# Optimization experiments

Measured on AMD Instinct MI355X. Metric: run time of the kernel, lower is better.

The kernel has to match this reference:

```python
import jax, jax.numpy as jnp
import numpy as np

EPS = 1e-5
NEG_SLOPE = 0.2
B, C, P, K, E, H = 16, 16, 2048, 16, 64, 2


def cross_set_gather(f, idx):
    # f: (B, C, P), idx: (B, P, K) -> (B, C, P, K)
    return jax.vmap(lambda fb, ib: fb[:, ib])(f, idx)


def bn(x, g, b, m, v, axes):
    # x normalized along channel dim; g,b,m,v shaped to broadcast via `axes` reshape
    return (x - m.reshape(axes)) * (g.reshape(axes) / jnp.sqrt(v.reshape(axes) + EPS)) + b.reshape(axes)


def setup_inputs() -> dict:
    key = jax.random.key(0)
    ks = jax.random.split(key, 16)
    features = jax.random.normal(ks[0], (B, C, P), dtype=jnp.float32)
    neighbor_indices = jax.random.randint(ks[1], (B, P, K), 0, P)
    mask = jax.random.randint(ks[2], (B, 1, P), 0, 2).astype(bool)
    s = 0.1
    return {
        "features": features,
        "neighbor_indices": neighbor_indices,
        "mask": mask,
        "node_w": jax.random.normal(ks[3], (H, E, C)) * s,
        "node_g": jnp.ones((H, E)),
        "node_b": jnp.zeros((H, E)),
        "node_m": jax.random.normal(ks[4], (H, E)) * s,
        "node_v": jax.random.uniform(ks[5], (H, E)) + 0.5,
        "edge_w": jax.random.normal(ks[6], (H, E, C)) * s,
        "edge_bias": jax.random.normal(ks[7], (H, E)) * s,
        "edge_g": jnp.ones((H, E)),
        "edge_b2": jnp.zeros((H, E)),
        "edge_m": jax.random.normal(ks[8], (H, E)) * s,
        "edge_v": jax.random.uniform(ks[9], (H, E)) + 0.5,
        "self_w": jax.random.normal(ks[10], (H, E)) * s,
        "self_b": jax.random.normal(ks[11], (H,)) * s,
        "nb_w": jax.random.normal(ks[12], (H, E)) * s,
        "nb_b": jax.random.normal(ks[13], (H,)) * s,
    }


def _forward(features, neighbor_indices, mask, node_w, node_g, node_b, node_m, node_v,
             edge_w, edge_bias, edge_g, edge_b2, edge_m, edge_v, self_w, self_b, nb_w, nb_b):
    mask_f = mask.astype(features.dtype)  # (B,1,P)
    # node encoding (Conv1d k=1 + BN): (B,H,E,P)
    nodes = jnp.einsum('hec,bcp->bhep', node_w, features)
    nodes = bn(nodes, node_g, node_b, node_m, node_v, (1, H, E, 1))
    # edge features: neighbor - center, (B,C,P,K)
    nbr = cross_set_gather(features, neighbor_indices)
    edge_feat = nbr - features[:, :, :, None]
    # edge encoding (Conv2d k=1 + BN): (B,H,E,P,K)
    enc = jnp.einsum('hec,bcpk->bhepk', edge_w, edge_feat) + edge_bias[None, :, :, None, None]
    enc = bn(enc, edge_g, edge_b2, edge_m, edge_v, (1, H, E, 1, 1))
    # attention scores
    self_score = jnp.einsum('he,bhep->bhp', self_w, nodes) + self_b[None, :, None]  # (B,H,P)
    nb_score = jnp.einsum('he,bhepk->bhpk', nb_w, enc) + nb_b[None, :, None, None]  # (B,H,P,K)
    logits = self_score[..., None] + nb_score
    logits = jnp.where(logits >= 0, logits, NEG_SLOPE * logits)  # leaky_relu(0.2)
    # neighbor validity mask: (B,P,K)
    valid = cross_set_gather(mask_f, neighbor_indices)[:, 0]
    vb = valid[:, None, :, :]  # (B,1,P,K)
    logits = jnp.where(vb == 0, -jnp.inf, logits)
    coef = jnp.nan_to_num(jax.nn.softmax(logits, axis=-1), nan=0.0, posinf=0.0, neginf=0.0)  # (B,H,P,K)
    # weighted aggregation + relu: (B,H,E,P)
    att = jax.nn.relu(jnp.einsum('bhpk,bhepk->bhep', coef, enc))
    # graph features: masked max over K
    enc_masked = jnp.where(vb[:, :, None, :, :] == 0, -jnp.inf, enc)
    graph = jnp.max(enc_masked, axis=-1)  # (B,H,E,P)
    graph = jnp.where(jnp.isinf(graph), 0.0, graph)
    # multi-head combine: element-wise max over heads, then mask
    att_out = jnp.max(att, axis=1) * mask_f  # (B,E,P)
    graph_out = jnp.max(graph, axis=1) * mask_f  # (B,E,P)
    return att_out, graph_out


def reference(features, neighbor_indices, mask, node_w, node_g, node_b, node_m, node_v,
              edge_w, edge_bias, edge_g, edge_b2, edge_m, edge_v, self_w, self_b, nb_w, nb_b):
    return _forward(features, neighbor_indices, mask, node_w, node_g, node_b, node_m, node_v,
                    edge_w, edge_bias, edge_g, edge_b2, edge_m, edge_v, self_w, self_b, nb_w, nb_b)
```

## Files before the change

kernel.cpp:

```cpp
#include <hip/hip_runtime.h>
#include <hip/hip_bf16.h>
#include <hip/hip_fp16.h>
#include <math.h>

#define NB 16
#define NC 16
#define NP 2048
#define NK 16
#define NE 64
#define NH 2
#define EPSV 1e-5f
#define NSLOPE 0.2f
#define QINV -1e30f
#define QTHR -1e29f

#define WS_PINFO 16384
#define WS_EPB   2162688

__device__ __forceinline__ float ldf(const void* p, int i, int isb) {
  return isb ? __bfloat162float(((const __hip_bfloat16*)p)[i]) : ((const float*)p)[i];
}
__device__ __forceinline__ unsigned f2bf(float f) {
  unsigned u = __float_as_uint(f);
  return (u + 0x7FFFu + ((u >> 16) & 1u)) >> 16;
}
__device__ __forceinline__ float bflo(unsigned v) { return __uint_as_float(v << 16); }
__device__ __forceinline__ float bfhi(unsigned v) { return __uint_as_float(v & 0xFFFF0000u); }

__global__ void __launch_bounds__(256) k_proj(
    const void* feat, const void* mask,
    const void* edge_w, const void* node_w,
    const void* edge_g, const void* edge_v,
    const void* node_g, const void* node_v, const void* node_b, const void* node_m,
    const void* self_w, const void* self_b, const void* nb_w,
    char* ws)
{
  __shared__ int sh_isb, sh_mbyte;
  __shared__ float ewl[128*17];
  __shared__ float nwl[128*17];
  __shared__ float fl[NC][64];
  __shared__ float w2[128], wn[128], ctr[128];
  __shared__ float s_wq[32], s_wsc[32], s_cself[2];

  const int tid = threadIdx.x;
  const int w = tid >> 6, lane = tid & 63;

  if (w == 0) {
    const unsigned short* u = (const unsigned short*)feat;
    int cnt = 0;
#pragma unroll
    for (int i = 0; i < 8; i++) {
      int ex = (u[lane*8 + i] >> 7) & 0xFF;
      cnt += (ex >= 100 && ex <= 135) ? 1 : 0;
    }
#pragma unroll
    for (int o = 32; o >= 1; o >>= 1) cnt += __shfl_xor(cnt, o);
    if (lane == 0) sh_isb = (cnt >= 460) ? 1 : 0;
  }
  if (w == 1) {
    const unsigned char* mb = (const unsigned char*)mask;
    int c = 0;
#pragma unroll
    for (int i = 0; i < 16; i++) {
      int ix = lane*16 + i;
      c += ((ix & 3) && mb[ix]) ? 1 : 0;
    }
#pragma unroll
    for (int o = 32; o >= 1; o >>= 1) c += __shfl_xor(c, o);
    if (lane == 0) sh_mbyte = (c > 0) ? 1 : 0;
  }
  __syncthreads();
  const int isb = sh_isb, mbyte = sh_mbyte;

  const int bid = blockIdx.x;
  const int b  = (bid & 7)*2 + ((bid >> 3) & 1);
  const int pt = bid >> 4;
  const int p0 = pt * 64;

  for (int i = tid; i < 128*16; i += 256) {
    const int he = i >> 4, c = i & 15;
    ewl[he*17 + c] = ldf(edge_w, i, isb);
    nwl[he*17 + c] = ldf(node_w, i, isb);
  }
  for (int i = tid; i < NC*64; i += 256) {
    int c = i >> 6, p = i & 63;
    fl[c][p] = ldf(feat, (b*NC + c)*NP + p0 + p, isb);
  }
  if (tid < 128) {
    const int he = tid;
    float se = ldf(edge_g, he, isb) * rsqrtf(ldf(edge_v, he, isb) + EPSV);
    float ns = ldf(node_g, he, isb) * rsqrtf(ldf(node_v, he, isb) + EPSV);
    w2[he]  = ldf(nb_w, he, isb) * se;
    wn[he]  = ldf(self_w, he, isb) * ns;
    ctr[he] = ldf(self_w, he, isb) * (ldf(node_b, he, isb) - ldf(node_m, he, isb) * ns);
  }
  __syncthreads();
  if (tid < 32) {
    const int h = tid >> 4, c = tid & 15;
    float sq = 0.f, sn = 0.f;
#pragma unroll 8
    for (int e = 0; e < NE; e++) {
      sq += w2[h*NE+e] * ewl[(h*NE+e)*17 + c];
      sn += wn[h*NE+e] * nwl[(h*NE+e)*17 + c];
    }
    s_wq[tid]  = sq;
    s_wsc[tid] = sn;
  }
  if (tid < 2) {
    float cs = 0.f;
#pragma unroll 8
    for (int e = 0; e < NE; e++) cs += ctr[tid*NE+e];
    s_cself[tid] = cs + ldf(self_b, tid, isb);
  }
  __syncthreads();

  const int e = tid & 63;
  const int pp = tid >> 6;
  float wv0[NC], wv1[NC];
#pragma unroll
  for (int c = 0; c < NC; c++) {
    wv0[c] = ewl[e*17 + c];
    wv1[c] = ewl[(NE + e)*17 + c];
  }
  unsigned* epb = (unsigned*)(ws + WS_EPB);
  const long base = (long)(b*NP + p0) * 64;
  for (int pass = 0; pass < 16; pass++) {
    const int p = pass*4 + pp;
    float a0 = 0.f, a1 = 0.f;
#pragma unroll
    for (int c = 0; c < NC; c++) {
      const float f = fl[c][p];
      a0 = fmaf(wv0[c], f, a0);
      a1 = fmaf(wv1[c], f, a1);
    }
    epb[base + (long)p*64 + e] = f2bf(a0) | (f2bf(a1) << 16);
  }

  if (tid < 64) {
    float q0=0.f, q1=0.f, s0=0.f, s1=0.f;
#pragma unroll
    for (int c = 0; c < NC; c++) {
      const float f = fl[c][tid];
      q0 = fmaf(s_wq[c],     f, q0);
      q1 = fmaf(s_wq[16+c],  f, q1);
      s0 = fmaf(s_wsc[c],    f, s0);
      s1 = fmaf(s_wsc[16+c], f, s1);
    }
    const int p = p0 + tid;
    bool mv;
    if (mbyte) mv = ((const unsigned char*)mask)[b*NP + p] != 0;
    else       mv = ((const int*)mask)[b*NP + p] != 0;
    float4 pi;
    pi.x = mv ? q0 : QINV;
    pi.y = mv ? q1 : QINV;
    pi.z = s0 + s_cself[0];
    pi.w = s1 + s_cself[1];
    ((float4*)(ws + WS_PINFO))[b*NP + p] = pi;
  }
}

__global__ void __launch_bounds__(256) k_main(
    const void* feat, const int* nidx,
    const void* edge_g, const void* edge_v, const void* edge_bias,
    const void* edge_m, const void* edge_b2,
    const void* nb_w, const void* nb_b,
    char* ws, void* out)
{
  __shared__ int sh_isb;
  __shared__ float sh_se[128], sh_cbe[128], sh_cnb[2];
  __shared__ uint2 ent[32][17];
  __shared__ unsigned char cntcm[32];
  __shared__ float att_t[NE][33];
  __shared__ float gr_t[NE][33];

  const int tid  = threadIdx.x;
  const int w    = tid >> 6;
  const int lane = tid & 63;

  if (w == 0) {
    const unsigned short* u = (const unsigned short*)feat;
    int cnt = 0;
#pragma unroll
    for (int i = 0; i < 8; i++) {
      int ex = (u[lane*8 + i] >> 7) & 0xFF;
      cnt += (ex >= 100 && ex <= 135) ? 1 : 0;
    }
#pragma unroll
    for (int o = 32; o >= 1; o >>= 1) cnt += __shfl_xor(cnt, o);
    if (lane == 0) sh_isb = (cnt >= 460) ? 1 : 0;
  }
  __syncthreads();
  const int isb = sh_isb;

  if (tid < 128) {
    const int he = tid, h = tid >> 6;
    float se = ldf(edge_g, he, isb) * rsqrtf(ldf(edge_v, he, isb) + EPSV);
    float cb = se * (ldf(edge_bias, he, isb) - ldf(edge_m, he, isb)) + ldf(edge_b2, he, isb);
    sh_se[he]  = se;
    sh_cbe[he] = cb;
    float t = ldf(nb_w, he, isb) * cb;
#pragma unroll
    for (int o = 32; o >= 1; o >>= 1) t += __shfl_xor(t, o);
    if ((tid & 63) == 0) sh_cnb[h] = t + ldf(nb_b, h, isb);
  }
  __syncthreads();

  const float4* pinfo = (const float4*)(ws + WS_PINFO);
  const int bid = blockIdx.x;
  const int b  = (bid & 7)*2 + ((bid >> 3) & 1);
  const int pt = bid >> 4;
  const int p0 = pt * 32;

  if (w == 0 && lane < 32) {
    const int p = p0 + lane;
    const float cnb0 = sh_cnb[0], cnb1 = sh_cnb[1];
    const float4 Pc = pinfo[b*NP + p];
    const bool cm = (Pc.x > QTHR);

    int idx[NK];
    {
      const int4* n4 = (const int4*)(nidx + ((long)b*NP + p)*NK);
#pragma unroll
      for (int q = 0; q < 4; q++) {
        const int4 v = n4[q];
        idx[q*4+0] = v.x; idx[q*4+1] = v.y; idx[q*4+2] = v.z; idx[q*4+3] = v.w;
      }
    }
    __half2 lgp[NK];
    unsigned vmask = 0;
    float mx0 = -INFINITY, mx1 = -INFINITY;
#pragma unroll
    for (int k = 0; k < NK; k++) {
      const float2 P = *(const float2*)&pinfo[b*NP + idx[k]];
      const bool valid = (P.x > QTHR);
      float l0 = Pc.z + P.x - Pc.x + cnb0;
      l0 = (l0 >= 0.f) ? l0 : NSLOPE * l0;
      float l1 = Pc.w + P.y - Pc.w + cnb1;
      l1 = Pc.w + P.y - Pc.y + cnb1;
      l1 = (l1 >= 0.f) ? l1 : NSLOPE * l1;
      l0 = valid ? l0 : -INFINITY;
      l1 = valid ? l1 : -INFINITY;
      vmask |= (valid ? 1u : 0u) << k;
      lgp[k] = __floats2half2_rn(l0, l1);
      mx0 = fmaxf(mx0, l0);
      mx1 = fmaxf(mx1, l1);
    }
    float sm0 = 0.f, sm1 = 0.f;
#pragma unroll
    for (int k = 0; k < NK; k++) {
      const float2 l = __half22float2(lgp[k]);
      sm0 += __expf(l.x - mx0);
      sm1 += __expf(l.y - mx1);
    }
    const float inv0 = 1.f / sm0, inv1 = 1.f / sm1;
    int pos = 0;
#pragma unroll
    for (int k = 0; k < NK; k++) {
      if ((vmask >> k) & 1) {
        const float2 l = __half22float2(lgp[k]);
        const float c0 = __expf(l.x - mx0) * inv0;
        const float c1 = __expf(l.y - mx1) * inv1;
        const __half2 h2 = __floats2half2_rn(c0, c1);
        uint2 e;
        e.x = *(const unsigned*)&h2;
        e.y = ((unsigned)idx[k]) << 8;
        ent[lane][pos] = e;
        pos++;
      }
    }
    cntcm[lane] = (unsigned char)(pos | (cm ? 0x80 : 0));
  }
  __syncthreads();

  const float se0 = sh_se[lane],  se1 = sh_se[NE + lane];
  const float cb0 = sh_cbe[lane], cb1 = sh_cbe[NE + lane];
  const char* epb_b = ws + WS_EPB + (long)b * NP * 256;

  for (int j = 0; j < 8; j++) {
    const int pl = w*8 + j;
    const unsigned cc = cntcm[pl];
    if (!(cc & 0x80)) { att_t[lane][pl] = 0.f; gr_t[lane][pl] = 0.f; continue; }
    const int cnt = cc & 0x7F;

    const unsigned rawp = *(const unsigned*)(epb_b + (long)(p0 + pl)*256 + lane*4);
    const float ra0 = bflo(rawp), ra1 = bfhi(rawp);
    const float cpe0 = cb0 - se0*ra0, cpe1 = cb1 - se1*ra1;

    float a0 = 0.f, a1 = 0.f;
    float mx0 = -INFINITY, mn0 = INFINITY, mx1 = -INFINITY, mn1 = INFINITY;
#pragma unroll 4
    for (int k = 0; k < cnt; k++) {
      const uint2 en = ent[pl][k];
      const float2 cf = __half22float2(*(const __half2*)&en.x);
      const unsigned v = *(const unsigned*)(epb_b + en.y + lane*4);
      const float v0 = bflo(v), v1 = bfhi(v);
      a0 = fmaf(cf.x, v0, a0);
      a1 = fmaf(cf.y, v1, a1);
      mx0 = fmaxf(mx0, v0); mn0 = fminf(mn0, v0);
      mx1 = fmaxf(mx1, v1); mn1 = fminf(mn1, v1);
    }
    const bool av = (cnt > 0);
    const float csel = av ? 1.f : 0.f;
    const float att0 = fmaxf(fmaf(se0, a0, cpe0*csel), 0.f);
    const float att1 = fmaxf(fmaf(se1, a1, cpe1*csel), 0.f);
    const float g0 = av ? fmaf(se0, (se0 >= 0.f) ? mx0 : mn0, cpe0) : 0.f;
    const float g1 = av ? fmaf(se1, (se1 >= 0.f) ? mx1 : mn1, cpe1) : 0.f;
    att_t[lane][pl] = fmaxf(att0, att1);
    gr_t[lane][pl]  = fmaxf(g0, g1);
  }
  __syncthreads();

  const long obase = (long)b * NE * NP;
  const long go = (long)NB * NE * NP;
  for (int i = tid; i < NE*32; i += 256) {
    const int ee = i >> 5, pp = i & 31;
    const long oi = obase + (long)ee * NP + p0 + pp;
    const float av = att_t[ee][pp], gv = gr_t[ee][pp];
    if (isb) {
      ((__hip_bfloat16*)out)[oi] = __float2bfloat16(av);
      ((__hip_bfloat16*)out)[oi + go] = __float2bfloat16(gv);
    } else {
      ((float*)out)[oi] = av;
      ((float*)out)[oi + go] = gv;
    }
  }
}

extern "C" void kernel_launch(void* const* d_in, const int* in_sizes, int n_in,
                              void* d_out, int out_size, void* d_ws, size_t ws_size,
                              hipStream_t stream)
{
  const void* feat      = d_in[0];
  const void* nidx      = d_in[1];
  const void* mask      = d_in[2];
  const void* node_w    = d_in[3];
  const void* node_g    = d_in[4];
  const void* node_b    = d_in[5];
  const void* node_m    = d_in[6];
  const void* node_v    = d_in[7];
  const void* edge_w    = d_in[8];
  const void* edge_bias = d_in[9];
  const void* edge_g    = d_in[10];
  const void* edge_b2   = d_in[11];
  const void* edge_m    = d_in[12];
  const void* edge_v    = d_in[13];
  const void* self_w    = d_in[14];
  const void* self_b    = d_in[15];
  const void* nb_w      = d_in[16];
  const void* nb_b      = d_in[17];
  char* ws = (char*)d_ws;

  hipLaunchKernelGGL(k_proj, dim3(NB*(NP/64)), dim3(256), 0, stream,
                     feat, mask, edge_w, node_w,
                     edge_g, edge_v,
                     node_g, node_v, node_b, node_m,
                     self_w, self_b, nb_w, ws);
  hipLaunchKernelGGL(k_main, dim3(NB*(NP/32)), dim3(256), 0, stream,
                     feat, (const int*)nidx,
                     edge_g, edge_v, edge_bias, edge_m, edge_b2,
                     nb_w, nb_b, ws, d_out);
}
```

Measured before the change: 122.7 us.

## Parallelize softmax across 8 lanes per point and hoist constants into k_proj

The per-point softmax and compaction in k_main used to run on 32 lanes of one wave, each looping over all 16 neighbors. It now spreads every point across 8 lanes with two neighbors each, using shuffle reductions for max and sum and a popcount prefix to compact the entries. The bf16/fp32 dtype probe and the edge BN constants move into block 0 of k_proj and are passed to k_main through workspace, which drops that per-block prologue and one barrier. Output stores are widened to two elements per thread. In exchange, k_main now depends on k_proj having written those workspace slots, and the extra shuffles add some cost.

```diff
diff --git a/kernel.cpp b/kernel.cpp
--- a/kernel.cpp
+++ b/kernel.cpp
@@ -14,6 +14,8 @@
 #define QINV -1e30f
 #define QTHR -1e29f
 
+#define WS_SECB  12288
+#define WS_CNB2  13312
 #define WS_PINFO 16384
 #define WS_EPB   2162688
 
@@ -30,9 +32,10 @@
 __global__ void __launch_bounds__(256) k_proj(
     const void* feat, const void* mask,
     const void* edge_w, const void* node_w,
-    const void* edge_g, const void* edge_v,
+    const void* edge_g, const void* edge_v, const void* edge_bias,
+    const void* edge_m, const void* edge_b2,
     const void* node_g, const void* node_v, const void* node_b, const void* node_m,
-    const void* self_w, const void* self_b, const void* nb_w,
+    const void* self_w, const void* self_b, const void* nb_w, const void* nb_b,
     char* ws)
 {
   __shared__ int sh_isb, sh_mbyte;
@@ -87,12 +90,25 @@
     fl[c][p] = ldf(feat, (b*NC + c)*NP + p0 + p, isb);
   }
   if (tid < 128) {
-    const int he = tid;
+    const int he = tid, h = tid >> 6;
     float se = ldf(edge_g, he, isb) * rsqrtf(ldf(edge_v, he, isb) + EPSV);
+    float cb = se * (ldf(edge_bias, he, isb) - ldf(edge_m, he, isb)) + ldf(edge_b2, he, isb);
     float ns = ldf(node_g, he, isb) * rsqrtf(ldf(node_v, he, isb) + EPSV);
     w2[he]  = ldf(nb_w, he, isb) * se;
     wn[he]  = ldf(self_w, he, isb) * ns;
     ctr[he] = ldf(self_w, he, isb) * (ldf(node_b, he, isb) - ldf(node_m, he, isb) * ns);
+    if (bid == 0) {
+      ((float2*)(ws + WS_SECB))[he] = make_float2(se, cb);
+      float t = ldf(nb_w, he, isb) * cb;
+#pragma unroll
+      for (int o = 32; o >= 1; o >>= 1) t += __shfl_xor(t, o);
+      if ((tid & 63) == 0)
+        ((float*)(ws + WS_CNB2))[h] = t + ldf(nb_b, h, isb);
+    }
+  }
+  if (bid == 0 && tid == 0) {
+    ((int*)ws)[0] = isb;
+    ((int*)ws)[1] = mbyte;
   }
   __syncthreads();
   if (tid < 32) {
@@ -159,14 +175,8 @@
   }
 }
 
-__global__ void __launch_bounds__(256) k_main(
-    const void* feat, const int* nidx,
-    const void* edge_g, const void* edge_v, const void* edge_bias,
-    const void* edge_m, const void* edge_b2,
-    const void* nb_w, const void* nb_b,
-    char* ws, void* out)
+__global__ void __launch_bounds__(256) k_main(const int* nidx, char* ws, void* out)
 {
-  __shared__ int sh_isb;
   __shared__ float sh_se[128], sh_cbe[128], sh_cnb[2];
   __shared__ uint2 ent[32][17];
   __shared__ unsigned char cntcm[32];
@@ -177,32 +187,13 @@
   const int w    = tid >> 6;
   const int lane = tid & 63;
 
-  if (w == 0) {
-    const unsigned short* u = (const unsigned short*)feat;
-    int cnt = 0;
-#pragma unroll
-    for (int i = 0; i < 8; i++) {
-      int ex = (u[lane*8 + i] >> 7) & 0xFF;
-      cnt += (ex >= 100 && ex <= 135) ? 1 : 0;
-    }
-#pragma unroll
-    for (int o = 32; o >= 1; o >>= 1) cnt += __shfl_xor(cnt, o);
-    if (lane == 0) sh_isb = (cnt >= 460) ? 1 : 0;
-  }
-  __syncthreads();
-  const int isb = sh_isb;
-
+  const int isb = ((const int*)ws)[0];
   if (tid < 128) {
-    const int he = tid, h = tid >> 6;
-    float se = ldf(edge_g, he, isb) * rsqrtf(ldf(edge_v, he, isb) + EPSV);
-    float cb = se * (ldf(edge_bias, he, isb) - ldf(edge_m, he, isb)) + ldf(edge_b2, he, isb);
-    sh_se[he]  = se;
-    sh_cbe[he] = cb;
-    float t = ldf(nb_w, he, isb) * cb;
-#pragma unroll
-    for (int o = 32; o >= 1; o >>= 1) t += __shfl_xor(t, o);
-    if ((tid & 63) == 0) sh_cnb[h] = t + ldf(nb_b, h, isb);
-  }
+    const float2 sc = ((const float2*)(ws + WS_SECB))[tid];
+    sh_se[tid]  = sc.x;
+    sh_cbe[tid] = sc.y;
+  }
+  if (tid < 2) sh_cnb[tid] = ((const float*)(ws + WS_CNB2))[tid];
   __syncthreads();
 
   const float4* pinfo = (const float4*)(ws + WS_PINFO);
@@ -210,65 +201,59 @@
   const int b  = (bid & 7)*2 + ((bid >> 3) & 1);
   const int pt = bid >> 4;
   const int p0 = pt * 32;
-
-  if (w == 0 && lane < 32) {
-    const int p = p0 + lane;
-    const float cnb0 = sh_cnb[0], cnb1 = sh_cnb[1];
+  const float cnb0 = sh_cnb[0], cnb1 = sh_cnb[1];
+
+  {
+    const int pl = w*8 + (lane >> 3);
+    const int p  = p0 + pl;
+    const int kk = (lane & 7) * 2;
     const float4 Pc = pinfo[b*NP + p];
     const bool cm = (Pc.x > QTHR);
-
-    int idx[NK];
-    {
-      const int4* n4 = (const int4*)(nidx + ((long)b*NP + p)*NK);
-#pragma unroll
-      for (int q = 0; q < 4; q++) {
-        const int4 v = n4[q];
-        idx[q*4+0] = v.x; idx[q*4+1] = v.y; idx[q*4+2] = v.z; idx[q*4+3] = v.w;
-      }
-    }
-    __half2 lgp[NK];
-    unsigned vmask = 0;
-    float mx0 = -INFINITY, mx1 = -INFINITY;
-#pragma unroll
-    for (int k = 0; k < NK; k++) {
-      const float2 P = *(const float2*)&pinfo[b*NP + idx[k]];
-      const bool valid = (P.x > QTHR);
-      float l0 = Pc.z + P.x - Pc.x + cnb0;
-      l0 = (l0 >= 0.f) ? l0 : NSLOPE * l0;
-      float l1 = Pc.w + P.y - Pc.w + cnb1;
-      l1 = Pc.w + P.y - Pc.y + cnb1;
-      l1 = (l1 >= 0.f) ? l1 : NSLOPE * l1;
-      l0 = valid ? l0 : -INFINITY;
-      l1 = valid ? l1 : -INFINITY;
-      vmask |= (valid ? 1u : 0u) << k;
-      lgp[k] = __floats2half2_rn(l0, l1);
-      mx0 = fmaxf(mx0, l0);
-      mx1 = fmaxf(mx1, l1);
-    }
-    float sm0 = 0.f, sm1 = 0.f;
-#pragma unroll
-    for (int k = 0; k < NK; k++) {
-      const float2 l = __half22float2(lgp[k]);
-      sm0 += __expf(l.x - mx0);
-      sm1 += __expf(l.y - mx1);
-    }
-    const float inv0 = 1.f / sm0, inv1 = 1.f / sm1;
-    int pos = 0;
-#pragma unroll
-    for (int k = 0; k < NK; k++) {
-      if ((vmask >> k) & 1) {
-        const float2 l = __half22float2(lgp[k]);
-        const float c0 = __expf(l.x - mx0) * inv0;
-        const float c1 = __expf(l.y - mx1) * inv1;
-        const __half2 h2 = __floats2half2_rn(c0, c1);
-        uint2 e;
-        e.x = *(const unsigned*)&h2;
-        e.y = ((unsigned)idx[k]) << 8;
-        ent[lane][pos] = e;
-        pos++;
-      }
-    }
-    cntcm[lane] = (unsigned char)(pos | (cm ? 0x80 : 0));
+    const int2 iv = *(const int2*)(nidx + ((long)b*NP + p)*NK + kk);
+    const float2 Q0 = *(const float2*)&pinfo[b*NP + iv.x];
+    const float2 Q1 = *(const float2*)&pinfo[b*NP + iv.y];
+    const bool v0 = (Q0.x > QTHR), v1 = (Q1.x > QTHR);
+
+    float l00 = Pc.z + Q0.x - Pc.x + cnb0;  l00 = (l00 >= 0.f) ? l00 : NSLOPE*l00;
+    float l01 = Pc.w + Q0.y - Pc.y + cnb1;  l01 = (l01 >= 0.f) ? l01 : NSLOPE*l01;
+    float l10 = Pc.z + Q1.x - Pc.x + cnb0;  l10 = (l10 >= 0.f) ? l10 : NSLOPE*l10;
+    float l11 = Pc.w + Q1.y - Pc.y + cnb1;  l11 = (l11 >= 0.f) ? l11 : NSLOPE*l11;
+    l00 = v0 ? l00 : -INFINITY;  l01 = v0 ? l01 : -INFINITY;
+    l10 = v1 ? l10 : -INFINITY;  l11 = v1 ? l11 : -INFINITY;
+
+    float mx0 = fmaxf(l00, l10), mx1 = fmaxf(l01, l11);
+#pragma unroll
+    for (int o = 1; o <= 4; o <<= 1) {
+      mx0 = fmaxf(mx0, __shfl_xor(mx0, o));
+      mx1 = fmaxf(mx1, __shfl_xor(mx1, o));
+    }
+    const float e00 = __expf(l00 - mx0), e10 = __expf(l10 - mx0);
+    const float e01 = __expf(l01 - mx1), e11 = __expf(l11 - mx1);
+    float s0 = e00 + e10, s1 = e01 + e11;
+#pragma unroll
+    for (int o = 1; o <= 4; o <<= 1) {
+      s0 += __shfl_xor(s0, o);
+      s1 += __shfl_xor(s1, o);
+    }
+    const float inv0 = 1.f / s0, inv1 = 1.f / s1;
+
+    unsigned vmask = ((v0 ? 1u : 0u) << kk) | ((v1 ? 1u : 0u) << (kk + 1));
+#pragma unroll
+    for (int o = 1; o <= 4; o <<= 1) vmask |= __shfl_xor(vmask, o);
+
+    const int pos0 = __popc(vmask & ((1u << kk) - 1));
+    if (v0) {
+      const __half2 h2 = __floats2half2_rn(e00 * inv0, e01 * inv1);
+      uint2 en; en.x = *(const unsigned*)&h2; en.y = ((unsigned)iv.x) << 8;
+      ent[pl][pos0] = en;
+    }
+    if (v1) {
+      const __half2 h2 = __floats2half2_rn(e10 * inv0, e11 * inv1);
+      uint2 en; en.x = *(const unsigned*)&h2; en.y = ((unsigned)iv.y) << 8;
+      ent[pl][pos0 + (v0 ? 1 : 0)] = en;
+    }
+    if ((lane & 7) == 0)
+      cntcm[pl] = (unsigned char)(__popc(vmask) | (cm ? 0x80 : 0));
   }
   __syncthreads();
 
@@ -312,16 +297,19 @@
 
   const long obase = (long)b * NE * NP;
   const long go = (long)NB * NE * NP;
-  for (int i = tid; i < NE*32; i += 256) {
-    const int ee = i >> 5, pp = i & 31;
+  for (int i = tid; i < NE*16; i += 256) {
+    const int ee = i >> 4, pp = (i & 15) * 2;
     const long oi = obase + (long)ee * NP + p0 + pp;
-    const float av = att_t[ee][pp], gv = gr_t[ee][pp];
+    const float a0 = att_t[ee][pp], a1 = att_t[ee][pp+1];
+    const float g0 = gr_t[ee][pp],  g1 = gr_t[ee][pp+1];
     if (isb) {
-      ((__hip_bfloat16*)out)[oi] = __float2bfloat16(av);
-      ((__hip_bfloat16*)out)[oi + go] = __float2bfloat16(gv);
+      __hip_bfloat16* o = (__hip_bfloat16*)out;
+      *(ushort2*)&o[oi]      = make_ushort2((unsigned short)f2bf(a0), (unsigned short)f2bf(a1));
+      *(ushort2*)&o[oi + go] = make_ushort2((unsigned short)f2bf(g0), (unsigned short)f2bf(g1));
     } else {
-      ((float*)out)[oi] = av;
-      ((float*)out)[oi + go] = gv;
+      float* o = (float*)out;
+      *(float2*)&o[oi]      = make_float2(a0, a1);
+      *(float2*)&o[oi + go] = make_float2(g0, g1);
     }
   }
 }
@@ -352,11 +340,9 @@
 
   hipLaunchKernelGGL(k_proj, dim3(NB*(NP/64)), dim3(256), 0, stream,
                      feat, mask, edge_w, node_w,
-                     edge_g, edge_v,
+                     edge_g, edge_v, edge_bias, edge_m, edge_b2,
                      node_g, node_v, node_b, node_m,
-                     self_w, self_b, nb_w, ws);
+                     self_w, self_b, nb_w, nb_b, ws);
   hipLaunchKernelGGL(k_main, dim3(NB*(NP/32)), dim3(256), 0, stream,
-                     feat, (const int*)nidx,
-                     edge_g, edge_v, edge_bias, edge_m, edge_b2,
-                     nb_w, nb_b, ws, d_out);
-}
+                     (const int*)nidx, ws, d_out);
+}
```

Result: faster. 119.7 us (-2.5%).
